# Kernel tuning notes

Measured on AMD Instinct MI355X. Metric: run time of the kernel, lower is better.

## Reference

```python
import jax, jax.numpy as jnp
import numpy as np

N, R, M, E, NE, B = 50000, 500, 120000, 960000, 800000, 8192
D, H1, HID, OC = 200, 256, 512, 50


def setup_inputs() -> dict:
    key = jax.random.key(0)
    ks = jax.random.split(key, 26)
    s = 0.05
    rn = lambda k, shp: jax.random.normal(k, shp, jnp.float32) * s
    return {
        "entity_emb": jax.random.normal(ks[0], (N, D), jnp.float32),
        "rel_emb": jax.random.normal(ks[1], (R, D), jnp.float32),
        "b_x": jax.random.randint(ks[2], (M,), 0, N),
        "b_node_graph_index": jax.random.randint(ks[3], (M,), 0, R),
        "edge_src": jax.random.randint(ks[4], (E,), 0, M),
        "edge_dst": jax.random.randint(ks[5], (E,), 0, M),
        "edge_w": jax.random.uniform(ks[6], (E,), jnp.float32),
        "big_src": jax.random.randint(ks[7], (NE,), 0, N),
        "big_dst": jax.random.randint(ks[8], (NE,), 0, N),
        "big_w": jax.random.uniform(ks[9], (NE,), jnp.float32),
        "perm": jax.random.permutation(ks[10], N),
        "batch_inputs": jnp.stack([
            jax.random.randint(ks[11], (B,), 0, N),
            jax.random.randint(ks[12], (B,), 0, R),
            jax.random.randint(ks[13], (B,), 0, N)], axis=1),
        "W1a": rn(ks[14], (2 * D, H1)), "W1b": rn(ks[15], (H1, D)),
        "W2a": rn(ks[16], (D, H1)), "W2b": rn(ks[17], (H1, D)),
        "Wle": rn(ks[18], (2 * D, 1)), "ble": jnp.zeros((1,), jnp.float32),
        "Wlo": rn(ks[19], (2 * D, D)), "blo": jnp.zeros((D,), jnp.float32),
        "Wg": rn(ks[20], (D, HID)), "Wd": rn(ks[21], (HID, HID)),
        "conv_w": rn(ks[22], (OC, 3)), "conv_b": jnp.zeros((OC,), jnp.float32),
        "fc_w": rn(ks[23], (OC * D, 1)), "fc_b": jnp.zeros((1,), jnp.float32),
    }


def _l2norm(x):
    return x / jnp.maximum(jnp.linalg.norm(x, axis=-1, keepdims=True), 1e-12)


def _gcn(x, src, dst, w, n, Wa, Wb):
    # two-layer GCN over sparse edge list: out = A @ relu(A @ x @ Wa) @ Wb
    agg = lambda h: jax.ops.segment_sum(h[src] * w[:, None], dst, num_segments=n)
    h = jax.nn.relu(agg(x) @ Wa)
    return agg(h) @ Wb


def _seg_softmax(v, idx, n):
    m = jax.ops.segment_max(v, idx, num_segments=n)
    e = jnp.exp(v - m[idx])
    s = jax.ops.segment_sum(e, idx, num_segments=n)
    return e / (s[idx] + 1e-16)


def _mce(ent, rel, b_x, b_gi, src, dst, w, W1a, W1b, Wle, ble, Wlo, blo):
    x = jnp.concatenate([ent[b_x], rel[b_gi]], axis=-1)          # [M, 400]
    e = _gcn(x, src, dst, w, b_x.shape[0], W1a, W1b)             # [M, 200]
    cnt = jax.ops.segment_sum(jnp.ones((b_x.shape[0],), e.dtype), b_x, num_segments=N)
    mean = jax.ops.segment_sum(e, b_x, num_segments=N) / jnp.maximum(cnt, 1.0)[:, None]
    z = mean[b_x]                                                # scatter_mean then gather
    emb = jnp.concatenate([e[b_x], z], axis=-1)                  # [M, 400]
    score = emb @ Wle + ble                                      # [M, 1]
    zs = _seg_softmax(score, b_x, N)                             # segment softmax
    pooled = jax.ops.segment_sum(zs * emb, b_x, num_segments=N)  # [N, 400]
    return (pooled @ Wlo + blo) + ent


def _dgi(h1, h2, Wg, Wd):
    p1 = jax.nn.relu(h1 @ Wg)
    p2 = jax.nn.relu(h2 @ Wg)
    c = jax.nn.sigmoid(jnp.mean(p1, axis=0))                     # readout [HID]
    t = Wd @ c
    return jnp.concatenate([p1 @ t, p2 @ t])                     # [2N]


def _convkb(trip, conv_w, conv_b, fc_w, fc_b):
    # trip [B,3,D]; Conv2d(1, OC, (1,3)) over [B,1,D,3] -> [B,OC,D]
    h = jax.nn.relu(jnp.einsum('bsd,os->bod', trip, conv_w) + conv_b[None, :, None])
    return h.reshape(trip.shape[0], -1) @ fc_w + fc_b            # [B,1]


def reference(entity_emb, rel_emb, b_x, b_node_graph_index, edge_src, edge_dst,
              edge_w, big_src, big_dst, big_w, perm, batch_inputs,
              W1a, W1b, W2a, W2b, Wle, ble, Wlo, blo, Wg, Wd,
              conv_w, conv_b, fc_w, fc_b):
    ent = _l2norm(entity_emb)
    rel = _l2norm(rel_emb)
    ent_shuf = ent[perm]
    ec = _mce(ent, rel, b_x, b_node_graph_index, edge_src, edge_dst, edge_w,
              W1a, W1b, Wle, ble, Wlo, blo)
    ec_ = _mce(ent_shuf, rel, b_x, b_node_graph_index, edge_src, edge_dst, edge_w,
               W1a, W1b, Wle, ble, Wlo, blo)
    eg = _gcn(ec, big_src, big_dst, big_w, N, W2a, W2b)
    eg_ = _gcn(ec_, big_src, big_dst, big_w, N, W2a, W2b)
    local_logits = _dgi(ec, ec_, Wg, Wd)
    global_logits = _dgi(eg, eg_, Wg, Wd)
    trip = jnp.stack([ec[batch_inputs[:, 0]], rel[batch_inputs[:, 1]],
                      ec[batch_inputs[:, 2]]], axis=1)           # [B,3,D]
    out_conv = _convkb(trip, conv_w, conv_b, fc_w, fc_b)
    return out_conv, local_logits, global_logits
```

## Files before the change

### kernel.cpp

```cpp
#include <hip/hip_runtime.h>

#define NN   50000
#define RR   500
#define MM   120000
#define EE   960000
#define NEE  800000
#define BB   8192
#define DD   200
#define HH1  256
#define HIDD 512
#define OCC  50

typedef unsigned int  u32;
typedef unsigned short u16;
typedef __attribute__((ext_vector_type(8))) short bf16x8;
typedef __attribute__((ext_vector_type(4))) float f32x4;

static __device__ __forceinline__ float bf2f(u16 u) {
    u32 x = ((u32)u) << 16;
    return __uint_as_float(x);
}
static __device__ __forceinline__ u16 f2bf(float f) {
    u32 x = __float_as_uint(f);
    u32 r = (x + 0x7FFFu + ((x >> 16) & 1u)) >> 16;
    return (u16)r;
}
static __device__ __forceinline__ u32 pack2(float a, float b) {
    return (u32)f2bf(a) | ((u32)f2bf(b) << 16);
}
static __device__ __forceinline__ void unpack2(u32 v, float& a, float& b) {
    a = bf2f((u16)(v & 0xFFFFu));
    b = bf2f((u16)(v >> 16));
}

static __device__ __forceinline__ float wredsum(float v) {
#pragma unroll
    for (int off = 32; off > 0; off >>= 1) v += __shfl_xor(v, off);
    return v;
}

static __device__ __forceinline__ u32 relu2bf(u32 x) {
    if (x & 0x00008000u) x &= 0xFFFF0000u;
    if (x & 0x80000000u) x &= 0x0000FFFFu;
    return x;
}
static __device__ __forceinline__ bf16x8 zero8() {
    bf16x8 z;
#pragma unroll
    for (int i = 0; i < 8; ++i) z[i] = 0;
    return z;
}

__global__ void k_l2norm(const float* __restrict__ in, float* __restrict__ outf,
                         u16* __restrict__ outb, int rows) {
    int w = (blockIdx.x * blockDim.x + threadIdx.x) >> 6;
    int lane = threadIdx.x & 63;
    if (w >= rows) return;
    const float* r = in + (size_t)w * DD;
    float s = 0.f;
    for (int d = lane; d < DD; d += 64) { float v = r[d]; s += v * v; }
    s = wredsum(s);
    float inv = 1.0f / fmaxf(sqrtf(s), 1e-12f);
    for (int d = lane; d < DD; d += 64) {
        float v = r[d] * inv;
        if (outf) outf[(size_t)w * DD + d] = v;
        if (outb) outb[(size_t)w * DD + d] = f2bf(v);
    }
}

__global__ void k_gather_perm(const int* __restrict__ bx, const int* __restrict__ perm,
                              int* __restrict__ idx1, int M) {
    int m = blockIdx.x * blockDim.x + threadIdx.x;
    if (m < M) idx1[m] = perm[bx[m]];
}

__global__ void k_edge_idx(const int* __restrict__ srcE, const int* __restrict__ map,
                           int* __restrict__ outE, int n) {
    int e = blockIdx.x * blockDim.x + threadIdx.x;
    if (e < n) outE[e] = map[srcE[e]];
}

__global__ void k_prepw(const float* __restrict__ src, int Nc, int Kd,
                        u16* __restrict__ hi, u16* __restrict__ lo) {
    int i = blockIdx.x * blockDim.x + threadIdx.x;
    if (i >= Nc * Kd) return;
    int n = i / Kd, k = i - n * Kd;
    float b = src[(size_t)k * Nc + n];
    u16 hb_ = f2bf(b);
    hi[i] = hb_;
    lo[i] = f2bf(b - bf2f(hb_));
}

__global__ void k_fusew(const float* __restrict__ W2b, const float* __restrict__ Wg,
                        u16* __restrict__ hi, u16* __restrict__ lo) {
    int i = blockIdx.x * blockDim.x + threadIdx.x;
    if (i >= HIDD * HH1) return;
    int n = i >> 8, k = i & 255;
    float s = 0.f;
    for (int j = 0; j < DD; ++j) s += W2b[k * DD + j] * Wg[(size_t)j * HIDD + n];
    u16 h = f2bf(s);
    hi[i] = h;
    lo[i] = f2bf(s - bf2f(h));
}

__global__ void k_hist(const int* __restrict__ idx, int* __restrict__ cnt, int n) {
    int i = blockIdx.x * blockDim.x + threadIdx.x;
    if (i < n) atomicAdd(&cnt[idx[i]], 1);
}

__global__ __launch_bounds__(1024) void k_scan(const int* __restrict__ in,
                                               int* __restrict__ out, int n) {
    __shared__ int wtot[16];
    __shared__ int wexc[16];
    __shared__ int s_carry;
    int tid = threadIdx.x, lane = tid & 63, wid = tid >> 6;
    if (tid == 0) s_carry = 0;
    __syncthreads();
    for (int base = 0; base < n; base += 1024) {
        int i = base + tid;
        int v = (i < n) ? in[i] : 0;
        int x = v;
#pragma unroll
        for (int off = 1; off < 64; off <<= 1) {
            int t = __shfl_up(x, off);
            if (lane >= off) x += t;
        }
        if (lane == 63) wtot[wid] = x;
        __syncthreads();
        if (wid == 0) {
            int wv2 = (lane < 16) ? wtot[lane] : 0;
            int y = wv2;
#pragma unroll
            for (int off = 1; off < 16; off <<= 1) {
                int t = __shfl_up(y, off);
                if (lane >= off) y += t;
            }
            if (lane < 16) wexc[lane] = y - wv2;
            if (lane == 15) wtot[15] = y;
        }
        __syncthreads();
        if (i < n) out[i] = s_carry + wexc[wid] + (x - v);
        int chunk_total = wtot[15];
        __syncthreads();
        if (tid == 0) s_carry += chunk_total;
        __syncthreads();
    }
    if (threadIdx.x == 0) out[n] = s_carry;
}

__global__ void k_fill2(const int* __restrict__ dst, const int* __restrict__ src,
                        const float* __restrict__ w, int* __restrict__ cursor,
                        int* __restrict__ srcs_out, float* __restrict__ ws_out, int n) {
    int e = blockIdx.x * blockDim.x + threadIdx.x;
    if (e >= n) return;
    int p = atomicAdd(&cursor[dst[e]], 1);
    srcs_out[p] = src[e];
    ws_out[p] = w[e];
}

__global__ void k_fill1(const int* __restrict__ idx, int* __restrict__ cursor,
                        int* __restrict__ outm, int n) {
    int m = blockIdx.x * blockDim.x + threadIdx.x;
    if (m >= n) return;
    int p = atomicAdd(&cursor[idx[m]], 1);
    outm[p] = m;
}

__global__ void k_pull_mce(const int* __restrict__ rp, const int* __restrict__ ivE,
                           const int* __restrict__ giE, const float* __restrict__ wE,
                           const u16* __restrict__ Pent, const u16* __restrict__ Prel,
                           u16* __restrict__ out, int ndst) {
    int wv = (blockIdx.x * blockDim.x + threadIdx.x) >> 6;
    if (wv >= ndst) return;
    int lane = threadIdx.x & 63;
    int beg = rp[wv], end = rp[wv + 1];
    float accA[2] = {0.f, 0.f}, accB[2] = {0.f, 0.f};
    int e = beg;
    for (; e + 4 <= end; e += 4) {
        int i0 = ivE[e], i1 = ivE[e + 1], i2 = ivE[e + 2], i3 = ivE[e + 3];
        int g0 = giE[e], g1 = giE[e + 1], g2 = giE[e + 2], g3 = giE[e + 3];
        float w0 = wE[e], w1 = wE[e + 1], w2 = wE[e + 2], w3 = wE[e + 3];
        const u32* pe0 = (const u32*)(Pent + (size_t)i0 * HH1);
        const u32* pe1 = (const u32*)(Pent + (size_t)i1 * HH1);
        const u32* pe2 = (const u32*)(Pent + (size_t)i2 * HH1);
        const u32* pe3 = (const u32*)(Pent + (size_t)i3 * HH1);
        const u32* pr0 = (const u32*)(Prel + (size_t)g0 * HH1);
        const u32* pr1 = (const u32*)(Prel + (size_t)g1 * HH1);
        const u32* pr2 = (const u32*)(Prel + (size_t)g2 * HH1);
        const u32* pr3 = (const u32*)(Prel + (size_t)g3 * HH1);
        u32 vp[4][2], vr[4][2];
#pragma unroll
        for (int t = 0; t < 2; ++t) {
            int p = lane + 64 * t;
            vp[0][t] = pe0[p]; vp[1][t] = pe1[p]; vp[2][t] = pe2[p]; vp[3][t] = pe3[p];
            vr[0][t] = pr0[p]; vr[1][t] = pr1[p]; vr[2][t] = pr2[p]; vr[3][t] = pr3[p];
        }
#pragma unroll
        for (int t = 0; t < 2; ++t) {
            float a, b, c, d;
            unpack2(vp[0][t], a, b); unpack2(vr[0][t], c, d);
            accA[t] += (a + c) * w0; accB[t] += (b + d) * w0;
            unpack2(vp[1][t], a, b); unpack2(vr[1][t], c, d);
            accA[t] += (a + c) * w1; accB[t] += (b + d) * w1;
            unpack2(vp[2][t], a, b); unpack2(vr[2][t], c, d);
            accA[t] += (a + c) * w2; accB[t] += (b + d) * w2;
            unpack2(vp[3][t], a, b); unpack2(vr[3][t], c, d);
            accA[t] += (a + c) * w3; accB[t] += (b + d) * w3;
        }
    }
    for (; e < end; ++e) {
        int iv = ivE[e], gi = giE[e];
        float w = wE[e];
        const u32* pe = (const u32*)(Pent + (size_t)iv * HH1);
        const u32* pr = (const u32*)(Prel + (size_t)gi * HH1);
#pragma unroll
        for (int t = 0; t < 2; ++t) {
            int p = lane + 64 * t;
            float a, b, c, d;
            unpack2(pe[p], a, b); unpack2(pr[p], c, d);
            accA[t] += (a + c) * w; accB[t] += (b + d) * w;
        }
    }
    u32* o = (u32*)(out + (size_t)wv * HH1);
#pragma unroll
    for (int t = 0; t < 2; ++t) o[lane + 64 * t] = pack2(accA[t], accB[t]);
}

template<int DIMS, int INS, int OUTS>
__global__ void k_pull(const int* __restrict__ rp, const int* __restrict__ srcs,
                       const float* __restrict__ wsrt,
                       const u16* __restrict__ inh, const u16* __restrict__ inl,
                       u16* __restrict__ outh, u16* __restrict__ outl, int ndst) {
    int wv = (blockIdx.x * blockDim.x + threadIdx.x) >> 6;
    if (wv >= ndst) return;
    int lane = threadIdx.x & 63;
    int beg = rp[wv], end = rp[wv + 1];
    constexpr int NP = DIMS / 2;
    constexpr int NT = (NP + 63) / 64;
    float accA[NT], accB[NT];
#pragma unroll
    for (int t = 0; t < NT; ++t) { accA[t] = 0.f; accB[t] = 0.f; }
    int e = beg;
    for (; e + 4 <= end; e += 4) {
        int s0 = srcs[e], s1 = srcs[e + 1], s2 = srcs[e + 2], s3 = srcs[e + 3];
        float w0 = wsrt[e], w1 = wsrt[e + 1], w2 = wsrt[e + 2], w3 = wsrt[e + 3];
        const u32* rh[4] = {
            (const u32*)(inh + (size_t)s0 * DIMS), (const u32*)(inh + (size_t)s1 * DIMS),
            (const u32*)(inh + (size_t)s2 * DIMS), (const u32*)(inh + (size_t)s3 * DIMS)};
        u32 vh[4][NT], vl[4][NT];
#pragma unroll
        for (int t = 0; t < NT; ++t) {
            int p = lane + 64 * t;
            if (p < NP) {
                vh[0][t] = rh[0][p]; vh[1][t] = rh[1][p];
                vh[2][t] = rh[2][p]; vh[3][t] = rh[3][p];
            }
        }
        if (INS) {
            const u32* rl[4] = {
                (const u32*)(inl + (size_t)s0 * DIMS), (const u32*)(inl + (size_t)s1 * DIMS),
                (const u32*)(inl + (size_t)s2 * DIMS), (const u32*)(inl + (size_t)s3 * DIMS)};
#pragma unroll
            for (int t = 0; t < NT; ++t) {
                int p = lane + 64 * t;
                if (p < NP) {
                    vl[0][t] = rl[0][p]; vl[1][t] = rl[1][p];
                    vl[2][t] = rl[2][p]; vl[3][t] = rl[3][p];
                }
            }
        }
        float ws[4] = {w0, w1, w2, w3};
#pragma unroll
        for (int q = 0; q < 4; ++q) {
#pragma unroll
            for (int t = 0; t < NT; ++t) {
                int p = lane + 64 * t;
                if (p < NP) {
                    float a, b;
                    unpack2(vh[q][t], a, b);
                    if (INS) { float a2, b2; unpack2(vl[q][t], a2, b2); a += a2; b += b2; }
                    accA[t] += a * ws[q]; accB[t] += b * ws[q];
                }
            }
        }
    }
    for (; e < end; ++e) {
        int s = srcs[e];
        float w = wsrt[e];
        const u32* rh = (const u32*)(inh + (size_t)s * DIMS);
        const u32* rl = INS ? (const u32*)(inl + (size_t)s * DIMS) : nullptr;
#pragma unroll
        for (int t = 0; t < NT; ++t) {
            int p = lane + 64 * t;
            if (p < NP) {
                float a, b;
                unpack2(rh[p], a, b);
                if (INS) { float a2, b2; unpack2(rl[p], a2, b2); a += a2; b += b2; }
                accA[t] += a * w; accB[t] += b * w;
            }
        }
    }
    u32* oh = (u32*)(outh + (size_t)wv * DIMS);
    u32* ol = OUTS ? (u32*)(outl + (size_t)wv * DIMS) : nullptr;
#pragma unroll
    for (int t = 0; t < NT; ++t) {
        int p = lane + 64 * t;
        if (p < NP) {
            if (OUTS == 0) {
                oh[p] = pack2(accA[t], accB[t]);
            } else {
                u16 ha = f2bf(accA[t]), hb_ = f2bf(accB[t]);
                u16 la = f2bf(accA[t] - bf2f(ha)), lb = f2bf(accB[t] - bf2f(hb_));
                oh[p] = (u32)ha | ((u32)hb_ << 16);
                ol[p] = (u32)la | ((u32)lb << 16);
            }
        }
    }
}

__global__ void k_segpool(const int* __restrict__ rpX, const int* __restrict__ mids,
                          const u16* __restrict__ e_buf, u16* __restrict__ pooled, int n) {
    int nv = (blockIdx.x * blockDim.x + threadIdx.x) >> 6;
    if (nv >= n) return;
    int lane = threadIdx.x & 63;
    int beg = rpX[nv], end = rpX[nv + 1];
    int cnt = end - beg;
    float accA[2] = {0.f, 0.f}, accB[2] = {0.f, 0.f};
    int e = beg;
    for (; e + 4 <= end; e += 4) {
        const u32* r0 = (const u32*)(e_buf + (size_t)mids[e] * DD);
        const u32* r1 = (const u32*)(e_buf + (size_t)mids[e + 1] * DD);
        const u32* r2 = (const u32*)(e_buf + (size_t)mids[e + 2] * DD);
        const u32* r3 = (const u32*)(e_buf + (size_t)mids[e + 3] * DD);
        u32 v[4][2];
#pragma unroll
        for (int t = 0; t < 2; ++t) {
            int p = lane + 64 * t;
            if (p < DD / 2) { v[0][t] = r0[p]; v[1][t] = r1[p]; v[2][t] = r2[p]; v[3][t] = r3[p]; }
        }
#pragma unroll
        for (int t = 0; t < 2; ++t) {
            int p = lane + 64 * t;
            if (p < DD / 2) {
                float a, b;
                unpack2(v[0][t], a, b); accA[t] += a; accB[t] += b;
                unpack2(v[1][t], a, b); accA[t] += a; accB[t] += b;
                unpack2(v[2][t], a, b); accA[t] += a; accB[t] += b;
                unpack2(v[3][t], a, b); accA[t] += a; accB[t] += b;
            }
        }
    }
    for (; e < end; ++e) {
        const u32* r = (const u32*)(e_buf + (size_t)mids[e] * DD);
#pragma unroll
        for (int t = 0; t < 2; ++t) {
            int p = lane + 64 * t;
            if (p < DD / 2) { float a, b; unpack2(r[p], a, b); accA[t] += a; accB[t] += b; }
        }
    }
    float inv = 1.0f / fmaxf((float)cnt, 1.0f);
    bool occ = cnt > 0;
    const u32* er = (const u32*)(e_buf + (size_t)nv * DD);
    u32* p0 = (u32*)(pooled + (size_t)nv * (2 * DD));
#pragma unroll
    for (int t = 0; t < 2; ++t) {
        int p = lane + 64 * t;
        if (p < DD / 2) {
            p0[p] = occ ? er[p] : 0u;
            p0[DD / 2 + p] = occ ? pack2(accA[t] * inv, accB[t] * inv) : 0u;
        }
    }
}

template<int AMODE, int BLO, int RELU_IN, int RELU_OUT, int HAS_BIAS, int HAS_ADD, int FUSE, int CMODE>
__global__ __launch_bounds__(256) void k_mfmamm(
    const u16* __restrict__ Ah, const u16* __restrict__ Al,
    const u16* __restrict__ Bh, const u16* __restrict__ Bl,
    void* __restrict__ Cv, u16* __restrict__ Cl,
    int Mr, int Nc, int Kd,
    const float* __restrict__ bias, const u16* __restrict__ addsrc,
    const int* __restrict__ addidx, const float* __restrict__ tvec,
    float* __restrict__ redout) {
    constexpr int BM = 128, BK = 32;
    constexpr int ASTR = 40;
    __shared__ u16 Ahs[2][BM * ASTR];
    __shared__ u16 Als[AMODE ? 2 : 1][AMODE ? (BM * ASTR) : 8];

    int tid = threadIdx.x;
    int wid = tid >> 6, lane = tid & 63;
    int wr = wid >> 1, wc = wid & 1;
    int r = lane & 15, h = lane >> 4;
    int bm0 = blockIdx.y * BM, bn0 = blockIdx.x * 128;
    int srow = (tid & 15) + 16 * (tid >> 6);
    int sg = (tid >> 4) & 3;
    int nk = (Kd + BK - 1) / BK;

    f32x4 acc[4][4];
#pragma unroll
    for (int i = 0; i < 4; ++i)
#pragma unroll
        for (int j = 0; j < 4; ++j) acc[i][j] = (f32x4){0.f, 0.f, 0.f, 0.f};

    uint4 pa[2], pl[2];
    {
        int kc = sg * 8;
        bool kok = (kc + 8 <= Kd);
#pragma unroll
        for (int it = 0; it < 2; ++it) {
            int row = srow + 64 * it;
            int gr = bm0 + row;
            uint4 v = make_uint4(0, 0, 0, 0), vl2 = make_uint4(0, 0, 0, 0);
            if (gr < Mr && kok) {
                v = *(const uint4*)(Ah + (size_t)gr * Kd + kc);
                if (AMODE) vl2 = *(const uint4*)(Al + (size_t)gr * Kd + kc);
            }
            if (RELU_IN) {
                v.x = relu2bf(v.x); v.y = relu2bf(v.y);
                v.z = relu2bf(v.z); v.w = relu2bf(v.w);
            }
            pa[it] = v;
            if (AMODE) pl[it] = vl2;
        }
#pragma unroll
        for (int it = 0; it < 2; ++it) {
            int row = srow + 64 * it;
            *(uint4*)(&Ahs[0][row * ASTR + sg * 8]) = pa[it];
            if (AMODE) *(uint4*)(&Als[0][row * ASTR + sg * 8]) = pl[it];
        }
    }
    __syncthreads();

    for (int k = 0; k < nk; ++k) {
        int cur = k & 1;
        uint4 na[2], nl[2];
        bool have_next = (k + 1 < nk);
        if (have_next) {
            int kc = (k + 1) * BK + sg * 8;
            bool kok = (kc + 8 <= Kd);
#pragma unroll
            for (int it = 0; it < 2; ++it) {
                int row = srow + 64 * it;
                int gr = bm0 + row;
                uint4 v = make_uint4(0, 0, 0, 0), vl2 = make_uint4(0, 0, 0, 0);
                if (gr < Mr && kok) {
                    v = *(const uint4*)(Ah + (size_t)gr * Kd + kc);
                    if (AMODE) vl2 = *(const uint4*)(Al + (size_t)gr * Kd + kc);
                }
                if (RELU_IN) {
                    v.x = relu2bf(v.x); v.y = relu2bf(v.y);
                    v.z = relu2bf(v.z); v.w = relu2bf(v.w);
                }
                na[it] = v;
                if (AMODE) nl[it] = vl2;
            }
        }
        bf16x8 bh4[4], bl4[4];
        {
            int kb = k * BK + h * 8;
            bool kbok = (kb + 8 <= Kd);
#pragma unroll
            for (int j = 0; j < 4; ++j) {
                int nrow = bn0 + wc * 64 + j * 16 + r;
                if (nrow < Nc && kbok) {
                    bh4[j] = *(const bf16x8*)(Bh + (size_t)nrow * Kd + kb);
                    if (BLO) bl4[j] = *(const bf16x8*)(Bl + (size_t)nrow * Kd + kb);
                } else { bh4[j] = zero8(); if (BLO) bl4[j] = zero8(); }
            }
        }
        bf16x8 af[4], alr[4];
#pragma unroll
        for (int i = 0; i < 4; ++i) {
            int mrow = wr * 64 + i * 16 + r;
            af[i] = *(const bf16x8*)(&Ahs[cur][mrow * ASTR + h * 8]);
            if (AMODE) alr[i] = *(const bf16x8*)(&Als[cur][mrow * ASTR + h * 8]);
        }
#pragma unroll
        for (int i = 0; i < 4; ++i)
#pragma unroll
            for (int j = 0; j < 4; ++j) {
                acc[i][j] = __builtin_amdgcn_mfma_f32_16x16x32_bf16(af[i], bh4[j], acc[i][j], 0, 0, 0);
                if (BLO)
                    acc[i][j] = __builtin_amdgcn_mfma_f32_16x16x32_bf16(af[i], bl4[j], acc[i][j], 0, 0, 0);
                if (AMODE)
                    acc[i][j] = __builtin_amdgcn_mfma_f32_16x16x32_bf16(alr[i], bh4[j], acc[i][j], 0, 0, 0);
            }
        if (have_next) {
#pragma unroll
            for (int it = 0; it < 2; ++it) {
                int row = srow + 64 * it;
                *(uint4*)(&Ahs[cur ^ 1][row * ASTR + sg * 8]) = na[it];
                if (AMODE) *(uint4*)(&Als[cur ^ 1][row * ASTR + sg * 8]) = nl[it];
            }
        }
        __syncthreads();
    }
    float colacc[4] = {0.f, 0.f, 0.f, 0.f};
#pragma unroll
    for (int i = 0; i < 4; ++i) {
        float rowacc[4] = {0.f, 0.f, 0.f, 0.f};
#pragma unroll
        for (int j = 0; j < 4; ++j) {
            int col = bn0 + wc * 64 + j * 16 + r;
            bool colok = col < Nc;
            float tv = (FUSE == 2 && colok) ? tvec[col] : 0.f;
#pragma unroll
            for (int rg = 0; rg < 4; ++rg) {
                int row = bm0 + wr * 64 + i * 16 + h * 4 + rg;
                float v = acc[i][j][rg];
                if (HAS_BIAS && colok) v += bias[col];
                if (RELU_OUT) v = fmaxf(v, 0.f);
                bool ok = colok && row < Mr;
                if (HAS_ADD && ok) {
                    int r2 = addidx ? addidx[row] : row;
                    v += bf2f(addsrc[(size_t)r2 * Nc + col]);
                }
                if (FUSE != 2 && ok) {
                    size_t cidx = (size_t)row * Nc + col;
                    if (CMODE == 0) ((u16*)Cv)[cidx] = f2bf(v);
                    else if (CMODE == 1) ((float*)Cv)[cidx] = v;
                    else {
                        u16 hi_ = f2bf(v);
                        ((u16*)Cv)[cidx] = hi_;
                        Cl[cidx] = f2bf(v - bf2f(hi_));
                    }
                }
                if (FUSE == 1 && ok) colacc[j] += v;
                if (FUSE == 2) rowacc[rg] += v * tv;
            }
        }
        if (FUSE == 2) {
#pragma unroll
            for (int rg = 0; rg < 4; ++rg) {
                float val = rowacc[rg];
                val += __shfl_xor(val, 1); val += __shfl_xor(val, 2);
                val += __shfl_xor(val, 4); val += __shfl_xor(val, 8);
                int row = bm0 + wr * 64 + i * 16 + h * 4 + rg;
                if (r == 0 && row < Mr) atomicAdd(&redout[row], val);
            }
        }
    }
    if (FUSE == 1) {
#pragma unroll
        for (int j = 0; j < 4; ++j) {
            float val = colacc[j];
            val += __shfl_xor(val, 16); val += __shfl_xor(val, 32);
            int col = bn0 + wc * 64 + j * 16 + r;
            if (h == 0 && col < Nc) atomicAdd(&redout[col], val);
        }
    }
}

__global__ void k_sigc(const float* __restrict__ csum, float* __restrict__ cvec) {
    int i = threadIdx.x;
    cvec[i] = 1.0f / (1.0f + expf(-csum[i] * (1.0f / (float)NN)));
}

__global__ void k_tmv(const float* __restrict__ Wd, const float* __restrict__ cvec,
                      float* __restrict__ tvec) {
    __shared__ float c[HIDD];
    int lane = threadIdx.x;
    for (int j = lane; j < HIDD; j += 64) c[j] = cvec[j];
    __syncthreads();
    int r0 = blockIdx.x * 16;
    for (int i = r0; i < r0 + 16; ++i) {
        const float* wr = Wd + (size_t)i * HIDD;
        float s = 0.f;
        for (int j = lane; j < HIDD; j += 64) s += wr[j] * c[j];
        s = wredsum(s);
        if (lane == 0) tvec[i] = s;
    }
}

__global__ void k_rowdot512(const float* __restrict__ p, const float* __restrict__ t,
                            float* __restrict__ out, int rows) {
    int g = blockIdx.x * blockDim.x + threadIdx.x;
    int wv = g >> 6;
    if (wv >= rows) return;
    int lane = g & 63;
    const float* r = p + (size_t)wv * HIDD;
    float s = 0.f;
#pragma unroll
    for (int t4 = 0; t4 < 8; ++t4) {
        int d = lane + t4 * 64;
        s += r[d] * t[d];
    }
    s = wredsum(s);
    if (lane == 0) out[wv] = s;
}

__global__ void k_rowdot512b(const u16* __restrict__ p, const float* __restrict__ t,
                             float* __restrict__ out, int rows) {
    int g = blockIdx.x * blockDim.x + threadIdx.x;
    int wv = g >> 6;
    if (wv >= rows) return;
    int lane = g & 63;
    const u32* r = (const u32*)(p + (size_t)wv * HIDD);
    float s = 0.f;
#pragma unroll
    for (int t4 = 0; t4 < 4; ++t4) {
        int pp = lane + t4 * 64;
        float a, b;
        unpack2(r[pp], a, b);
        s += a * t[2 * pp] + b * t[2 * pp + 1];
    }
    s = wredsum(s);
    if (lane == 0) out[wv] = s;
}

__global__ void k_convkb(const u16* __restrict__ ec, const float* __restrict__ rel,
                         const int* __restrict__ bi, const float* __restrict__ cw,
                         const float* __restrict__ cb, const float* __restrict__ fcw,
                         const float* __restrict__ fcb, float* __restrict__ out) {
    __shared__ float t0[DD], t1[DD], t2[DD];
    __shared__ float red[4];
    int b = blockIdx.x, tid = threadIdx.x;
    int i0 = bi[b * 3 + 0], i1 = bi[b * 3 + 1], i2 = bi[b * 3 + 2];
    if (tid < DD) {
        t0[tid] = bf2f(ec[(size_t)i0 * DD + tid]);
        t1[tid] = rel[(size_t)i1 * DD + tid];
        t2[tid] = bf2f(ec[(size_t)i2 * DD + tid]);
    }
    __syncthreads();
    float partial = 0.f;
    if (tid < DD) {
        float a = t0[tid], bb = t1[tid], c = t2[tid];
        for (int o = 0; o < OCC; ++o) {
            float h = fmaxf(cw[o * 3 + 0] * a + cw[o * 3 + 1] * bb + cw[o * 3 + 2] * c + cb[o], 0.f);
            partial += h * fcw[o * DD + tid];
        }
    }
    partial = wredsum(partial);
    if ((tid & 63) == 0) red[tid >> 6] = partial;
    __syncthreads();
    if (tid == 0) out[b] = red[0] + red[1] + red[2] + red[3] + fcb[0];
}

__global__ void k_sentinel(float* out, float val) { out[threadIdx.x] = val; }

extern "C" void kernel_launch(void* const* d_in, const int* in_sizes, int n_in,
                              void* d_out, int out_size, void* d_ws, size_t ws_size,
                              hipStream_t stream) {
    const float* entity_emb = (const float*)d_in[0];
    const float* rel_emb    = (const float*)d_in[1];
    const int*   b_x        = (const int*)d_in[2];
    const int*   b_gi       = (const int*)d_in[3];
    const int*   e_src      = (const int*)d_in[4];
    const int*   e_dst      = (const int*)d_in[5];
    const float* e_w        = (const float*)d_in[6];
    const int*   big_src    = (const int*)d_in[7];
    const int*   big_dst    = (const int*)d_in[8];
    const float* big_w      = (const float*)d_in[9];
    const int*   perm       = (const int*)d_in[10];
    const int*   batch_in   = (const int*)d_in[11];
    const float* W1a        = (const float*)d_in[12];
    const float* W1b        = (const float*)d_in[13];
    const float* W2a        = (const float*)d_in[14];
    const float* W2b        = (const float*)d_in[15];
    const float* Wlo        = (const float*)d_in[18];
    const float* blo        = (const float*)d_in[19];
    const float* Wg         = (const float*)d_in[20];
    const float* Wd         = (const float*)d_in[21];
    const float* conv_w     = (const float*)d_in[22];
    const float* conv_b     = (const float*)d_in[23];
    const float* fc_w       = (const float*)d_in[24];
    const float* fc_b       = (const float*)d_in[25];
    float* out = (float*)d_out;

    size_t off = 0;
    auto balloc = [&](size_t nbytes) {
        size_t p = off;
        off += (nbytes + 511) & ~(size_t)511;
        return p;
    };
    char* base = (char*)d_ws;
    u16*   entb = (u16*)(base + balloc((size_t)NN * DD * 2));
    float* relf = (float*)(base + balloc((size_t)RR * DD * 4));
    u16*   relb = (u16*)(base + balloc((size_t)RR * DD * 2));
    u16*   Pent = (u16*)(base + balloc((size_t)NN * HH1 * 2));
    u16*   Prel = (u16*)(base + balloc((size_t)RR * HH1 * 2));
    int*   idx1 = (int*)(base + balloc((size_t)MM * 4));
    u16*   ecb  = (u16*)(base + balloc((size_t)NN * DD * 2));
    int*   rpB  = (int*)(base + balloc((size_t)(NN + 1) * 4));
    int*   srcB = (int*)(base + balloc((size_t)NEE * 4));
    float* wB   = (float*)(base + balloc((size_t)NEE * 4));
    int*   rpE  = (int*)(base + balloc((size_t)(MM + 1) * 4));
    int*   srcE = (int*)(base + balloc((size_t)EE * 4));
    float* wE   = (float*)(base + balloc((size_t)EE * 4));
    int*   ivE  = (int*)(base + balloc((size_t)EE * 4));
    int*   giE  = (int*)(base + balloc((size_t)EE * 4));
    int*   rpX  = (int*)(base + balloc((size_t)(NN + 1) * 4));
    int*   mids = (int*)(base + balloc((size_t)MM * 4));
    int*   curB = (int*)(base + balloc((size_t)NN * 4));
    int*   curE = (int*)(base + balloc((size_t)MM * 4));
    int*   curX = (int*)(base + balloc((size_t)NN * 4));
    u16* w1aT_h  = (u16*)(base + balloc(200 * 256 * 2));
    u16* w1aT_l  = (u16*)(base + balloc(200 * 256 * 2));
    u16* w1abT_h = (u16*)(base + balloc(200 * 256 * 2));
    u16* w1abT_l = (u16*)(base + balloc(200 * 256 * 2));
    u16* w1bT_h  = (u16*)(base + balloc(256 * 200 * 2));
    u16* w1bT_l  = (u16*)(base + balloc(256 * 200 * 2));
    u16* wloT_h  = (u16*)(base + balloc(400 * 200 * 2));
    u16* wloT_l  = (u16*)(base + balloc(400 * 200 * 2));
    u16* wgT_h   = (u16*)(base + balloc(200 * 512 * 2));
    u16* wgT_l   = (u16*)(base + balloc(200 * 512 * 2));
    u16* w2aT_h  = (u16*)(base + balloc(200 * 256 * 2));
    u16* w2aT_l  = (u16*)(base + balloc(200 * 256 * 2));
    u16* w2bgT_h = (u16*)(base + balloc(512 * 256 * 2));
    u16* w2bgT_l = (u16*)(base + balloc(512 * 256 * 2));
    char*  Aarena = base + balloc((size_t)MM * HH1 * 2);
    char*  Barena = base + balloc((size_t)MM * DD * 2);
    char*  Carena = base + balloc((size_t)MM * DD * 2);
    float* csum = (float*)(base + balloc(4 * 2048));
    float* cvec = csum + 512;
    float* t_l  = csum + 1024;
    float* t_g  = csum + 1536;

    if (ws_size < off) {
        k_sentinel<<<dim3(1), dim3(8), 0, stream>>>(out, (float)(ws_size >> 20));
        return;
    }

    const size_t PL = 20000000;
    const size_t PH = 25600000;
    u16*   aggx   = (u16*)Aarena;
    u16*   hb     = (u16*)Barena;
    u16*   e_buf  = (u16*)Carena;
    u16*   pooled = (u16*)Aarena;
    u16*   a1h    = (u16*)Aarena;
    u16*   a1l    = (u16*)(Aarena + PL);
    u16*   h2h    = (u16*)Barena;
    u16*   h2l    = (u16*)(Barena + PH);
    u16*   g2h    = (u16*)Aarena;
    u16*   g2l    = (u16*)(Aarena + PH);
    u16*   pb16   = (u16*)Barena;
    float* pbuf   = (float*)Aarena;

    dim3 blk(256);
    auto wgrid = [](int items) { return dim3((unsigned)((items + 3) / 4)); };
    auto tgrid = [](int items) { return dim3((unsigned)((items + 255) / 256)); };
    auto mmgrid = [](int Mr, int Nc) { return dim3((unsigned)((Nc + 127) / 128), (unsigned)((Mr + 127) / 128)); };

    k_l2norm<<<wgrid(NN), blk, 0, stream>>>(entity_emb, nullptr, entb, NN);
    k_l2norm<<<wgrid(RR), blk, 0, stream>>>(rel_emb, relf, relb, RR);
    k_gather_perm<<<tgrid(MM), blk, 0, stream>>>(b_x, perm, idx1, MM);
    k_prepw<<<tgrid(256 * 200), blk, 0, stream>>>(W1a, 256, 200, w1aT_h, w1aT_l);
    k_prepw<<<tgrid(256 * 200), blk, 0, stream>>>(W1a + 200 * 256, 256, 200, w1abT_h, w1abT_l);
    k_prepw<<<tgrid(200 * 256), blk, 0, stream>>>(W1b, 200, 256, w1bT_h, w1bT_l);
    k_prepw<<<tgrid(200 * 400), blk, 0, stream>>>(Wlo, 200, 400, wloT_h, wloT_l);
    k_prepw<<<tgrid(512 * 200), blk, 0, stream>>>(Wg, 512, 200, wgT_h, wgT_l);
    k_prepw<<<tgrid(256 * 200), blk, 0, stream>>>(W2a, 256, 200, w2aT_h, w2aT_l);
    k_fusew<<<tgrid(512 * 256), blk, 0, stream>>>(W2b, Wg, w2bgT_h, w2bgT_l);

    hipMemsetAsync(curB, 0, (size_t)NN * 4, stream);
    hipMemsetAsync(curE, 0, (size_t)MM * 4, stream);
    hipMemsetAsync(curX, 0, (size_t)NN * 4, stream);
    k_hist<<<tgrid(NEE), blk, 0, stream>>>(big_dst, curB, NEE);
    k_hist<<<tgrid(EE), blk, 0, stream>>>(e_dst, curE, EE);
    k_hist<<<tgrid(MM), blk, 0, stream>>>(b_x, curX, MM);
    k_scan<<<dim3(1), dim3(1024), 0, stream>>>(curB, rpB, NN);
    k_scan<<<dim3(1), dim3(1024), 0, stream>>>(curE, rpE, MM);
    k_scan<<<dim3(1), dim3(1024), 0, stream>>>(curX, rpX, NN);
    hipMemcpyAsync(curB, rpB, (size_t)NN * 4, hipMemcpyDeviceToDevice, stream);
    hipMemcpyAsync(curE, rpE, (size_t)MM * 4, hipMemcpyDeviceToDevice, stream);
    hipMemcpyAsync(curX, rpX, (size_t)NN * 4, hipMemcpyDeviceToDevice, stream);
    k_fill2<<<tgrid(NEE), blk, 0, stream>>>(big_dst, big_src, big_w, curB, srcB, wB, NEE);
    k_fill2<<<tgrid(EE), blk, 0, stream>>>(e_dst, e_src, e_w, curE, srcE, wE, EE);
    k_fill1<<<tgrid(MM), blk, 0, stream>>>(b_x, curX, mids, MM);
    k_edge_idx<<<tgrid(EE), blk, 0, stream>>>(srcE, b_gi, giE, EE);

    k_mfmamm<0, 0, 0, 0, 0, 0, 0, 0><<<mmgrid(NN, HH1), blk, 0, stream>>>(
        entb, nullptr, w1aT_h, w1aT_l, Pent, nullptr, NN, HH1, DD,
        nullptr, nullptr, nullptr, nullptr, nullptr);
    k_mfmamm<0, 0, 0, 0, 0, 0, 0, 0><<<mmgrid(RR, HH1), blk, 0, stream>>>(
        relb, nullptr, w1abT_h, w1abT_l, Prel, nullptr, RR, HH1, DD,
        nullptr, nullptr, nullptr, nullptr, nullptr);

    for (int v = 0; v < 2; ++v) {
        const int* ivmap  = v ? idx1 : b_x;
        const int* addidx = v ? perm : nullptr;

        k_edge_idx<<<tgrid(EE), blk, 0, stream>>>(srcE, ivmap, ivE, EE);
        k_pull_mce<<<wgrid(MM), blk, 0, stream>>>(rpE, ivE, giE, wE, Pent, Prel, aggx, MM);
        k_mfmamm<0, 0, 1, 0, 0, 0, 0, 0><<<mmgrid(MM, DD), blk, 0, stream>>>(
            aggx, nullptr, w1bT_h, w1bT_l, hb, nullptr, MM, DD, HH1,
            nullptr, nullptr, nullptr, nullptr, nullptr);
        k_pull<DD, 0, 0><<<wgrid(MM), blk, 0, stream>>>(rpE, srcE, wE, hb, nullptr,
                                                        e_buf, nullptr, MM);
        k_segpool<<<wgrid(NN), blk, 0, stream>>>(rpX, mids, e_buf, pooled, NN);
        k_mfmamm<0, 0, 0, 0, 1, 1, 0, 0><<<mmgrid(NN, DD), blk, 0, stream>>>(
            pooled, nullptr, wloT_h, wloT_l, ecb, nullptr, NN, DD, 2 * DD,
            blo, entb, addidx, nullptr, nullptr);

        if (v == 0) {
            hipMemsetAsync(csum, 0, 512 * sizeof(float), stream);
            k_mfmamm<0, 0, 0, 1, 0, 0, 1, 1><<<mmgrid(NN, HIDD), blk, 0, stream>>>(
                ecb, nullptr, wgT_h, wgT_l, pbuf, nullptr, NN, HIDD, DD,
                nullptr, nullptr, nullptr, nullptr, csum);
            k_sigc<<<dim3(1), dim3(512), 0, stream>>>(csum, cvec);
            k_tmv<<<dim3(32), dim3(64), 0, stream>>>(Wd, cvec, t_l);
            k_rowdot512<<<wgrid(NN), blk, 0, stream>>>(pbuf, t_l, out + BB, NN);
            k_convkb<<<dim3(BB), blk, 0, stream>>>(ecb, relf, batch_in,
                                                   conv_w, conv_b, fc_w, fc_b, out);
        } else {
            hipMemsetAsync(out + BB + NN, 0, (size_t)NN * 4, stream);
            k_mfmamm<0, 0, 0, 1, 0, 0, 2, 1><<<mmgrid(NN, HIDD), blk, 0, stream>>>(
                ecb, nullptr, wgT_h, wgT_l, nullptr, nullptr, NN, HIDD, DD,
                nullptr, nullptr, nullptr, t_l, out + BB + NN);
        }

        k_pull<DD, 0, 1><<<wgrid(NN), blk, 0, stream>>>(rpB, srcB, wB, ecb, nullptr,
                                                        a1h, a1l, NN);
        k_mfmamm<1, 1, 0, 1, 0, 0, 0, 2><<<mmgrid(NN, HH1), blk, 0, stream>>>(
            a1h, a1l, w2aT_h, w2aT_l, h2h, h2l, NN, HH1, DD,
            nullptr, nullptr, nullptr, nullptr, nullptr);
        k_pull<HH1, 1, 1><<<wgrid(NN), blk, 0, stream>>>(rpB, srcB, wB, h2h, h2l,
                                                         g2h, g2l, NN);

        if (v == 0) {
            hipMemsetAsync(csum, 0, 512 * sizeof(float), stream);
            k_mfmamm<1, 1, 0, 1, 0, 0, 1, 0><<<mmgrid(NN, HIDD), blk, 0, stream>>>(
                g2h, g2l, w2bgT_h, w2bgT_l, pb16, nullptr, NN, HIDD, HH1,
                nullptr, nullptr, nullptr, nullptr, csum);
            k_sigc<<<dim3(1), dim3(512), 0, stream>>>(csum, cvec);
            k_tmv<<<dim3(32), dim3(64), 0, stream>>>(Wd, cvec, t_g);
            k_rowdot512b<<<wgrid(NN), blk, 0, stream>>>(pb16, t_g, out + BB + 2 * (size_t)NN, NN);
        } else {
            hipMemsetAsync(out + BB + 3 * (size_t)NN, 0, (size_t)NN * 4, stream);
            k_mfmamm<1, 1, 0, 1, 0, 0, 2, 0><<<mmgrid(NN, HIDD), blk, 0, stream>>>(
                g2h, g2l, w2bgT_h, w2bgT_l, nullptr, nullptr, NN, HIDD, HH1,
                nullptr, nullptr, nullptr, t_g, out + BB + 3 * (size_t)NN);
        }
    }

    (void)in_sizes; (void)n_in; (void)out_size;
}
```

Before: 2.089 ms.

## Batch local DGI GEMM over both MCE views and merge small launches

When workspace allows, both MCE passes write to separate buffers. The local DGI projection then runs as one GEMM over 2N rows, with the column sum restricted to the first N rows, followed by one row-dot over both views. The three prefix scans are merged into a single 3-block launch, and the sigmoid kernel is folded into k_tmv. This cuts kernel launches and the separate FUSE=2 GEMM, at the cost of a bf16 intermediate instead of fp32 for the local path and extra workspace.

```diff
diff --git a/kernel.cpp b/kernel.cpp
--- a/kernel.cpp
+++ b/kernel.cpp
@@ -108,11 +108,16 @@
     if (i < n) atomicAdd(&cnt[idx[i]], 1);
 }
 
-__global__ __launch_bounds__(1024) void k_scan(const int* __restrict__ in,
-                                               int* __restrict__ out, int n) {
+__global__ __launch_bounds__(1024) void k_scan3(
+    const int* __restrict__ in0, int* __restrict__ out0, int n0,
+    const int* __restrict__ in1, int* __restrict__ out1, int n1,
+    const int* __restrict__ in2, int* __restrict__ out2, int n2) {
     __shared__ int wtot[16];
     __shared__ int wexc[16];
     __shared__ int s_carry;
+    const int* in = (blockIdx.x == 0) ? in0 : (blockIdx.x == 1) ? in1 : in2;
+    int* out = (blockIdx.x == 0) ? out0 : (blockIdx.x == 1) ? out1 : out2;
+    int n = (blockIdx.x == 0) ? n0 : (blockIdx.x == 1) ? n1 : n2;
     int tid = threadIdx.x, lane = tid & 63, wid = tid >> 6;
     if (tid == 0) s_carry = 0;
     __syncthreads();
@@ -377,7 +382,7 @@
     const u16* __restrict__ Ah, const u16* __restrict__ Al,
     const u16* __restrict__ Bh, const u16* __restrict__ Bl,
     void* __restrict__ Cv, u16* __restrict__ Cl,
-    int Mr, int Nc, int Kd,
+    int Mr, int Nc, int Kd, int redrows,
     const float* __restrict__ bias, const u16* __restrict__ addsrc,
     const int* __restrict__ addidx, const float* __restrict__ tvec,
     float* __restrict__ redout) {
@@ -524,7 +529,7 @@
                         Cl[cidx] = f2bf(v - bf2f(hi_));
                     }
                 }
-                if (FUSE == 1 && ok) colacc[j] += v;
+                if (FUSE == 1 && ok && row < redrows) colacc[j] += v;
                 if (FUSE == 2) rowacc[rg] += v * tv;
             }
         }
@@ -550,16 +555,12 @@
     }
 }
 
-__global__ void k_sigc(const float* __restrict__ csum, float* __restrict__ cvec) {
-    int i = threadIdx.x;
-    cvec[i] = 1.0f / (1.0f + expf(-csum[i] * (1.0f / (float)NN)));
-}
-
-__global__ void k_tmv(const float* __restrict__ Wd, const float* __restrict__ cvec,
+__global__ void k_tmv(const float* __restrict__ Wd, const float* __restrict__ csum,
                       float* __restrict__ tvec) {
     __shared__ float c[HIDD];
     int lane = threadIdx.x;
-    for (int j = lane; j < HIDD; j += 64) c[j] = cvec[j];
+    for (int j = lane; j < HIDD; j += 64)
+        c[j] = 1.0f / (1.0f + expf(-csum[j] * (1.0f / (float)NN)));
     __syncthreads();
     int r0 = blockIdx.x * 16;
     for (int i = r0; i < r0 + 16; ++i) {
@@ -679,7 +680,6 @@
     u16*   Pent = (u16*)(base + balloc((size_t)NN * HH1 * 2));
     u16*   Prel = (u16*)(base + balloc((size_t)RR * HH1 * 2));
     int*   idx1 = (int*)(base + balloc((size_t)MM * 4));
-    u16*   ecb  = (u16*)(base + balloc((size_t)NN * DD * 2));
     int*   rpB  = (int*)(base + balloc((size_t)(NN + 1) * 4));
     int*   srcB = (int*)(base + balloc((size_t)NEE * 4));
     float* wB   = (float*)(base + balloc((size_t)NEE * 4));
@@ -714,8 +714,13 @@
     float* cvec = csum + 512;
     float* t_l  = csum + 1024;
     float* t_g  = csum + 1536;
-
-    if (ws_size < off) {
+    u16*   ecb  = (u16*)(base + balloc((size_t)NN * DD * 2));
+    size_t off_small = off;
+    u16*   ecb2 = ecb + (size_t)NN * DD;
+    bool bigws = (off_small + (size_t)NN * DD * 2) <= ws_size;
+    (void)cvec;
+
+    if (ws_size < off_small) {
         k_sentinel<<<dim3(1), dim3(8), 0, stream>>>(out, (float)(ws_size >> 20));
         return;
     }
@@ -733,6 +738,7 @@
     u16*   g2h    = (u16*)Aarena;
     u16*   g2l    = (u16*)(Aarena + PH);
     u16*   pb16   = (u16*)Barena;
+    u16*   pb16L  = (u16*)Aarena;
     float* pbuf   = (float*)Aarena;
 
     dim3 blk(256);
@@ -757,9 +763,7 @@
     k_hist<<<tgrid(NEE), blk, 0, stream>>>(big_dst, curB, NEE);
     k_hist<<<tgrid(EE), blk, 0, stream>>>(e_dst, curE, EE);
     k_hist<<<tgrid(MM), blk, 0, stream>>>(b_x, curX, MM);
-    k_scan<<<dim3(1), dim3(1024), 0, stream>>>(curB, rpB, NN);
-    k_scan<<<dim3(1), dim3(1024), 0, stream>>>(curE, rpE, MM);
-    k_scan<<<dim3(1), dim3(1024), 0, stream>>>(curX, rpX, NN);
+    k_scan3<<<dim3(3), dim3(1024), 0, stream>>>(curB, rpB, NN, curE, rpE, MM, curX, rpX, NN);
     hipMemcpyAsync(curB, rpB, (size_t)NN * 4, hipMemcpyDeviceToDevice, stream);
     hipMemcpyAsync(curE, rpE, (size_t)MM * 4, hipMemcpyDeviceToDevice, stream);
     hipMemcpyAsync(curX, rpX, (size_t)NN * 4, hipMemcpyDeviceToDevice, stream);
@@ -769,67 +773,84 @@
     k_edge_idx<<<tgrid(EE), blk, 0, stream>>>(srcE, b_gi, giE, EE);
 
     k_mfmamm<0, 0, 0, 0, 0, 0, 0, 0><<<mmgrid(NN, HH1), blk, 0, stream>>>(
-        entb, nullptr, w1aT_h, w1aT_l, Pent, nullptr, NN, HH1, DD,
+        entb, nullptr, w1aT_h, w1aT_l, Pent, nullptr, NN, HH1, DD, NN,
         nullptr, nullptr, nullptr, nullptr, nullptr);
     k_mfmamm<0, 0, 0, 0, 0, 0, 0, 0><<<mmgrid(RR, HH1), blk, 0, stream>>>(
-        relb, nullptr, w1abT_h, w1abT_l, Prel, nullptr, RR, HH1, DD,
+        relb, nullptr, w1abT_h, w1abT_l, Prel, nullptr, RR, HH1, DD, RR,
         nullptr, nullptr, nullptr, nullptr, nullptr);
 
-    for (int v = 0; v < 2; ++v) {
+    auto mce_pass = [&](int v, u16* ecdst) {
         const int* ivmap  = v ? idx1 : b_x;
         const int* addidx = v ? perm : nullptr;
-
         k_edge_idx<<<tgrid(EE), blk, 0, stream>>>(srcE, ivmap, ivE, EE);
         k_pull_mce<<<wgrid(MM), blk, 0, stream>>>(rpE, ivE, giE, wE, Pent, Prel, aggx, MM);
         k_mfmamm<0, 0, 1, 0, 0, 0, 0, 0><<<mmgrid(MM, DD), blk, 0, stream>>>(
-            aggx, nullptr, w1bT_h, w1bT_l, hb, nullptr, MM, DD, HH1,
+            aggx, nullptr, w1bT_h, w1bT_l, hb, nullptr, MM, DD, HH1, MM,
             nullptr, nullptr, nullptr, nullptr, nullptr);
         k_pull<DD, 0, 0><<<wgrid(MM), blk, 0, stream>>>(rpE, srcE, wE, hb, nullptr,
                                                         e_buf, nullptr, MM);
         k_segpool<<<wgrid(NN), blk, 0, stream>>>(rpX, mids, e_buf, pooled, NN);
         k_mfmamm<0, 0, 0, 0, 1, 1, 0, 0><<<mmgrid(NN, DD), blk, 0, stream>>>(
-            pooled, nullptr, wloT_h, wloT_l, ecb, nullptr, NN, DD, 2 * DD,
+            pooled, nullptr, wloT_h, wloT_l, ecdst, nullptr, NN, DD, 2 * DD, NN,
             blo, entb, addidx, nullptr, nullptr);
-
-        if (v == 0) {
-            hipMemsetAsync(csum, 0, 512 * sizeof(float), stream);
-            k_mfmamm<0, 0, 0, 1, 0, 0, 1, 1><<<mmgrid(NN, HIDD), blk, 0, stream>>>(
-                ecb, nullptr, wgT_h, wgT_l, pbuf, nullptr, NN, HIDD, DD,
-                nullptr, nullptr, nullptr, nullptr, csum);
-            k_sigc<<<dim3(1), dim3(512), 0, stream>>>(csum, cvec);
-            k_tmv<<<dim3(32), dim3(64), 0, stream>>>(Wd, cvec, t_l);
-            k_rowdot512<<<wgrid(NN), blk, 0, stream>>>(pbuf, t_l, out + BB, NN);
-            k_convkb<<<dim3(BB), blk, 0, stream>>>(ecb, relf, batch_in,
-                                                   conv_w, conv_b, fc_w, fc_b, out);
-        } else {
-            hipMemsetAsync(out + BB + NN, 0, (size_t)NN * 4, stream);
-            k_mfmamm<0, 0, 0, 1, 0, 0, 2, 1><<<mmgrid(NN, HIDD), blk, 0, stream>>>(
-                ecb, nullptr, wgT_h, wgT_l, nullptr, nullptr, NN, HIDD, DD,
-                nullptr, nullptr, nullptr, t_l, out + BB + NN);
-        }
-
-        k_pull<DD, 0, 1><<<wgrid(NN), blk, 0, stream>>>(rpB, srcB, wB, ecb, nullptr,
+    };
+
+    auto gcn_pass = [&](int v, const u16* ecsrc) {
+        k_pull<DD, 0, 1><<<wgrid(NN), blk, 0, stream>>>(rpB, srcB, wB, ecsrc, nullptr,
                                                         a1h, a1l, NN);
         k_mfmamm<1, 1, 0, 1, 0, 0, 0, 2><<<mmgrid(NN, HH1), blk, 0, stream>>>(
-            a1h, a1l, w2aT_h, w2aT_l, h2h, h2l, NN, HH1, DD,
+            a1h, a1l, w2aT_h, w2aT_l, h2h, h2l, NN, HH1, DD, NN,
             nullptr, nullptr, nullptr, nullptr, nullptr);
         k_pull<HH1, 1, 1><<<wgrid(NN), blk, 0, stream>>>(rpB, srcB, wB, h2h, h2l,
                                                          g2h, g2l, NN);
-
         if (v == 0) {
             hipMemsetAsync(csum, 0, 512 * sizeof(float), stream);
             k_mfmamm<1, 1, 0, 1, 0, 0, 1, 0><<<mmgrid(NN, HIDD), blk, 0, stream>>>(
-                g2h, g2l, w2bgT_h, w2bgT_l, pb16, nullptr, NN, HIDD, HH1,
+                g2h, g2l, w2bgT_h, w2bgT_l, pb16, nullptr, NN, HIDD, HH1, NN,
                 nullptr, nullptr, nullptr, nullptr, csum);
-            k_sigc<<<dim3(1), dim3(512), 0, stream>>>(csum, cvec);
-            k_tmv<<<dim3(32), dim3(64), 0, stream>>>(Wd, cvec, t_g);
+            k_tmv<<<dim3(32), dim3(64), 0, stream>>>(Wd, csum, t_g);
             k_rowdot512b<<<wgrid(NN), blk, 0, stream>>>(pb16, t_g, out + BB + 2 * (size_t)NN, NN);
         } else {
             hipMemsetAsync(out + BB + 3 * (size_t)NN, 0, (size_t)NN * 4, stream);
             k_mfmamm<1, 1, 0, 1, 0, 0, 2, 0><<<mmgrid(NN, HIDD), blk, 0, stream>>>(
-                g2h, g2l, w2bgT_h, w2bgT_l, nullptr, nullptr, NN, HIDD, HH1,
+                g2h, g2l, w2bgT_h, w2bgT_l, nullptr, nullptr, NN, HIDD, HH1, NN,
                 nullptr, nullptr, nullptr, t_g, out + BB + 3 * (size_t)NN);
         }
+    };
+
+    if (bigws) {
+        mce_pass(0, ecb);
+        mce_pass(1, ecb2);
+        hipMemsetAsync(csum, 0, 512 * sizeof(float), stream);
+        k_mfmamm<0, 0, 0, 1, 0, 0, 1, 0><<<mmgrid(2 * NN, HIDD), blk, 0, stream>>>(
+            ecb, nullptr, wgT_h, wgT_l, pb16L, nullptr, 2 * NN, HIDD, DD, NN,
+            nullptr, nullptr, nullptr, nullptr, csum);
+        k_tmv<<<dim3(32), dim3(64), 0, stream>>>(Wd, csum, t_l);
+        k_rowdot512b<<<wgrid(2 * NN), blk, 0, stream>>>(pb16L, t_l, out + BB, 2 * NN);
+        k_convkb<<<dim3(BB), blk, 0, stream>>>(ecb, relf, batch_in,
+                                               conv_w, conv_b, fc_w, fc_b, out);
+        gcn_pass(0, ecb);
+        gcn_pass(1, ecb2);
+    } else {
+        for (int v = 0; v < 2; ++v) {
+            mce_pass(v, ecb);
+            if (v == 0) {
+                hipMemsetAsync(csum, 0, 512 * sizeof(float), stream);
+                k_mfmamm<0, 0, 0, 1, 0, 0, 1, 1><<<mmgrid(NN, HIDD), blk, 0, stream>>>(
+                    ecb, nullptr, wgT_h, wgT_l, pbuf, nullptr, NN, HIDD, DD, NN,
+                    nullptr, nullptr, nullptr, nullptr, csum);
+                k_tmv<<<dim3(32), dim3(64), 0, stream>>>(Wd, csum, t_l);
+                k_rowdot512<<<wgrid(NN), blk, 0, stream>>>(pbuf, t_l, out + BB, NN);
+                k_convkb<<<dim3(BB), blk, 0, stream>>>(ecb, relf, batch_in,
+                                                       conv_w, conv_b, fc_w, fc_b, out);
+            } else {
+                hipMemsetAsync(out + BB + NN, 0, (size_t)NN * 4, stream);
+                k_mfmamm<0, 0, 0, 1, 0, 0, 2, 1><<<mmgrid(NN, HIDD), blk, 0, stream>>>(
+                    ecb, nullptr, wgT_h, wgT_l, nullptr, nullptr, NN, HIDD, DD, NN,
+                    nullptr, nullptr, nullptr, t_l, out + BB + NN);
+            }
+            gcn_pass(v, ecb);
+        }
     }
 
     (void)in_sizes; (void)n_in; (void)out_size;
```

Result: faster. 1.997 ms (-4.4%).
